# Kernel tuning notes

Hardware: AMD Instinct MI355X
Metric: run time of the kernel (lower is better)

Reference implementation:

```python
import jax, jax.numpy as jnp
import numpy as np

N_NODES = 8192
N_GRAPHS = 16
KNN_K = 80
N_FEAT = 6
KNN_COLS = (0, 1, 2, 3)
HID = 128
HID6 = 6 * HID
N_LABELS = 3
BN_EPS = 1e-5


def knn_edges(pos, batch, k):
    # pos: [N, 4]; batch: [N] graph ids. Returns (src, tgt) with k neighbors per node,
    # restricted to same graph, excluding self (PyG knn_graph, flow source_to_target).
    n = pos.shape[0]
    sq = jnp.sum(pos * pos, axis=1)
    d2 = sq[:, None] + sq[None, :] - 2.0 * (pos @ pos.T)  # [N, N]
    valid = (batch[:, None] == batch[None, :]) & ~jnp.eye(n, dtype=bool)
    d2 = jnp.where(valid, d2, jnp.inf)
    _, idx = jax.lax.top_k(-d2, k)  # k smallest distances per row
    src = idx.reshape(-1)                      # neighbor j (message source)
    tgt = jnp.repeat(jnp.arange(n), k)         # center node i (message target)
    return src, tgt


def tag_conv(x, src, tgt, norm, W, b):
    # TAGConv K=2: out = sum_k (A_hat^k x) W_k + b, A_hat = D^-1/2 A D^-1/2
    n = x.shape[0]
    out = x @ W[0]
    h = x
    for k in range(1, W.shape[0]):
        h = jax.ops.segment_sum(norm[:, None] * h[src], tgt, num_segments=n)
        out = out + h @ W[k]
    return out + b


def pool_mean_max(x, batch, n_graphs):
    cnt = jax.ops.segment_sum(jnp.ones((x.shape[0],), x.dtype), batch, num_segments=n_graphs)
    mean = jax.ops.segment_sum(x, batch, num_segments=n_graphs) / cnt[:, None]
    mx = jax.ops.segment_max(x, batch, num_segments=n_graphs)
    return jnp.concatenate([mean, mx], axis=1)


def setup_inputs() -> dict:
    key = jax.random.key(0)
    ks = jax.random.split(key, 16)
    x = jax.random.normal(ks[0], (N_NODES, N_FEAT), dtype=jnp.float32)
    batch = jnp.repeat(jnp.arange(N_GRAPHS, dtype=jnp.int32), N_NODES // N_GRAPHS)
    s1 = 1.0 / np.sqrt(N_FEAT)
    s2 = 1.0 / np.sqrt(HID)
    s3 = 1.0 / np.sqrt(HID6)
    return {
        "x": x,
        "batch": batch,
        "conv1_w": jax.random.uniform(ks[1], (3, N_FEAT, HID), jnp.float32, -s1, s1),
        "conv1_b": jnp.zeros((HID,), jnp.float32),
        "conv2_w": jax.random.uniform(ks[2], (3, HID, HID), jnp.float32, -s2, s2),
        "conv2_b": jnp.zeros((HID,), jnp.float32),
        "conv3_w": jax.random.uniform(ks[3], (3, HID, HID), jnp.float32, -s2, s2),
        "conv3_b": jnp.zeros((HID,), jnp.float32),
        "bn_gamma": jnp.ones((HID6,), jnp.float32),
        "bn_beta": jnp.zeros((HID6,), jnp.float32),
        "bn_mean": 0.1 * jax.random.normal(ks[4], (HID6,), jnp.float32),
        "bn_var": jax.random.uniform(ks[5], (HID6,), jnp.float32, 0.5, 1.5),
        "lin_w": jax.random.uniform(ks[6], (5, HID6, HID6), jnp.float32, -s3, s3),
        "lin_b": jax.random.uniform(ks[7], (5, HID6), jnp.float32, -s3, s3),
        "out_w": jax.random.uniform(ks[8], (HID6, N_LABELS), jnp.float32, -s3, s3),
        "out_b": jax.random.uniform(ks[9], (N_LABELS,), jnp.float32, -s3, s3),
    }


def reference(x, batch, conv1_w, conv1_b, conv2_w, conv2_b, conv3_w, conv3_b,
              bn_gamma, bn_beta, bn_mean, bn_var, lin_w, lin_b, out_w, out_b):
    n = x.shape[0]
    pos = x[:, jnp.array(KNN_COLS)]
    src, tgt = knn_edges(pos, batch, KNN_K)
    # gcn_norm without self loops (edge dropout disabled: eval-mode determinism)
    deg = jax.ops.segment_sum(jnp.ones_like(src, dtype=x.dtype), tgt, num_segments=n)
    dinv = jnp.where(deg > 0, jax.lax.rsqrt(jnp.maximum(deg, 1.0)), 0.0)
    norm = dinv[src] * dinv[tgt]

    h = jax.nn.leaky_relu(tag_conv(x, src, tgt, norm, conv1_w, conv1_b))
    p1 = pool_mean_max(h, batch, N_GRAPHS)
    h = jax.nn.leaky_relu(tag_conv(h, src, tgt, norm, conv2_w, conv2_b))
    p2 = pool_mean_max(h, batch, N_GRAPHS)
    h = jax.nn.leaky_relu(tag_conv(h, src, tgt, norm, conv3_w, conv3_b))
    p3 = pool_mean_max(h, batch, N_GRAPHS)

    g = jnp.concatenate([p1, p2, p3], axis=1)  # [B, 768]
    g = (g - bn_mean) * jax.lax.rsqrt(bn_var + BN_EPS) * bn_gamma + bn_beta
    for i in range(lin_w.shape[0]):
        g = jax.nn.leaky_relu(g @ lin_w[i] + lin_b[i])
    out = g @ out_w + out_b
    return out.reshape(-1, N_LABELS)
```

## Files before the change

kernel.cpp:

```cpp
#include <hip/hip_runtime.h>

constexpr int N    = 8192;
constexpr int NPG  = 512;
constexpr int NG   = 16;
constexpr int KNN  = 80;
constexpr int F0   = 6;
constexpr int HID  = 128;
constexpr int H6   = 768;
constexpr int RPB  = 16;
constexpr int BPGR = NPG / RPB;

__device__ __forceinline__ float leaky(float v) { return v > 0.0f ? v : 0.01f * v; }

__device__ __forceinline__ int lanes_below(unsigned long long m) {
    return __builtin_amdgcn_mbcnt_hi((unsigned)(m >> 32),
           __builtin_amdgcn_mbcnt_lo((unsigned)m, 0));
}

__device__ __forceinline__ int wave_count_sum(int c) {
    int total = 0;
    #pragma unroll
    for (int b = 0; b < 4; b++)
        total += (int)__popcll(__ballot((c >> b) & 1)) << b;
    return total;
}

__global__ __launch_bounds__(256) void knn_kernel(const float* __restrict__ x,
                                                  int* __restrict__ nbr) {
    constexpr int BPG = 128;
    const int tid  = threadIdx.x;
    const int lane = tid & 63;
    const int wv   = tid >> 6;
    const int base = (blockIdx.x / BPG) << 9;
    const int t    = base + (blockIdx.x & (BPG - 1)) * 4 + wv;
    const int tl   = t - base;

    __shared__ float px[512], py[512], pz[512], pw[512];
    __shared__ unsigned long long skey[4 * 128];

    for (int j = tid; j < 512; j += 256) {
        const float* row = x + (size_t)(base + j) * F0;
        const float2 ra = *(const float2*)(row);
        const float2 rb = *(const float2*)(row + 2);
        px[j] = ra.x; py[j] = ra.y; pz[j] = rb.x; pw[j] = rb.y;
    }
    __syncthreads();

    const float tx = px[tl], ty = py[tl], tz = pz[tl], tw = pw[tl];
    const float sqt = tx*tx + ty*ty + tz*tz + tw*tw;

    unsigned d2m[8];
    #pragma unroll
    for (int j = 0; j < 8; j++) {
        const int node = j * 64 + lane;
        const float jx = px[node], jy = py[node], jz = pz[node], jw = pw[node];
        const float sqj = jx*jx + jy*jy + jz*jz + jw*jw;
        const float dot = tx*jx + ty*jy + tz*jz + tw*jw;
        const float d2  = sqt + sqj - 2.0f * dot;
        unsigned u = __float_as_uint(d2);
        u = (u & 0x80000000u) ? ~u : (u | 0x80000000u);
        d2m[j] = (node == tl) ? 0xFFFFFFFFu : u;
    }

    unsigned V = 0;
    for (int b = 31; b >= 0; --b) {
        const unsigned test = V | (1u << b);
        int c = 0;
        #pragma unroll
        for (int j = 0; j < 8; j++) c += (d2m[j] < test) ? 1 : 0;
        if (wave_count_sum(c) < KNN) V = test;
    }

    int c = 0;
    #pragma unroll
    for (int j = 0; j < 8; j++) c += (d2m[j] < V) ? 1 : 0;
    const int n_lt = wave_count_sum(c);
    const int need = KNN - n_lt;

    const int woff = wv * 128;
    int cnt_total = 0, taken = 0;
    #pragma unroll
    for (int j = 0; j < 8; j++) {
        const bool lt = d2m[j] < V;
        const bool eq = d2m[j] == V;
        const unsigned long long meq = __ballot(eq);
        const bool sel = lt || (eq && (taken + lanes_below(meq)) < need);
        taken += (int)__popcll(meq);
        const unsigned long long msel = __ballot(sel);
        if (sel) {
            const int pos = cnt_total + lanes_below(msel);
            skey[woff + pos] = ((unsigned long long)d2m[j] << 32)
                             | (unsigned)(base + j * 64 + lane);
        }
        cnt_total += (int)__popcll(msel);
    }
    for (int i = KNN + lane; i < 128; i += 64) skey[woff + i] = ~0ULL;
    __syncthreads();

    for (int kk = 2; kk <= 128; kk <<= 1) {
        for (int jj = kk >> 1; jj >= 1; jj >>= 1) {
            const int i  = ((lane & ~(jj - 1)) << 1) | (lane & (jj - 1));
            const int ix = i | jj;
            const unsigned long long a = skey[woff + i];
            const unsigned long long b = skey[woff + ix];
            const bool up = ((i & kk) == 0);
            if ((a > b) == up) { skey[woff + i] = b; skey[woff + ix] = a; }
            __syncthreads();
        }
    }

    if (lane < KNN)      nbr[t * KNN + lane]      = (int)(unsigned)skey[woff + lane];
    if (lane + 64 < KNN) nbr[t * KNN + lane + 64] = (int)(unsigned)skey[woff + lane + 64];
}

__global__ __launch_bounds__(256) void prop6(const float* __restrict__ hin,
                                             const int* __restrict__ nbr,
                                             float* __restrict__ hout) {
    const int t = blockIdx.x * 256 + threadIdx.x;
    if (t >= N) return;
    const int* nb = nbr + t * KNN;
    float a0=0.f,a1=0.f,a2=0.f,a3=0.f,a4=0.f,a5=0.f;
    for (int i = 0; i < KNN; i += 4) {
        const int4 s4 = *(const int4*)(nb + i);
        {   const float* r = hin + (size_t)s4.x * F0;
            a0+=r[0]; a1+=r[1]; a2+=r[2]; a3+=r[3]; a4+=r[4]; a5+=r[5]; }
        {   const float* r = hin + (size_t)s4.y * F0;
            a0+=r[0]; a1+=r[1]; a2+=r[2]; a3+=r[3]; a4+=r[4]; a5+=r[5]; }
        {   const float* r = hin + (size_t)s4.z * F0;
            a0+=r[0]; a1+=r[1]; a2+=r[2]; a3+=r[3]; a4+=r[4]; a5+=r[5]; }
        {   const float* r = hin + (size_t)s4.w * F0;
            a0+=r[0]; a1+=r[1]; a2+=r[2]; a3+=r[3]; a4+=r[4]; a5+=r[5]; }
    }
    const float inv = 1.0f / 80.0f;
    float* o = hout + (size_t)t * F0;
    o[0]=a0*inv; o[1]=a1*inv; o[2]=a2*inv; o[3]=a3*inv; o[4]=a4*inv; o[5]=a5*inv;
}

__global__ __launch_bounds__(128) void prop128(const float* __restrict__ hin,
                                               const int* __restrict__ nbr,
                                               float* __restrict__ hout) {
    const int lane = threadIdx.x & 31;
    const int t    = blockIdx.x * 4 + (threadIdx.x >> 5);
    const int* nb  = nbr + t * KNN;
    float a0=0.f,a1=0.f,a2=0.f,a3=0.f;
    for (int i = 0; i < KNN; i += 16) {
        const int4 sA = *(const int4*)(nb + i);
        const int4 sB = *(const int4*)(nb + i + 4);
        const int4 sC = *(const int4*)(nb + i + 8);
        const int4 sD = *(const int4*)(nb + i + 12);
        const int idx[16] = {sA.x,sA.y,sA.z,sA.w, sB.x,sB.y,sB.z,sB.w,
                             sC.x,sC.y,sC.z,sC.w, sD.x,sD.y,sD.z,sD.w};
        float4 v[16];
        #pragma unroll
        for (int q = 0; q < 16; q++)
            v[q] = *(const float4*)(hin + (size_t)idx[q] * HID + lane * 4);
        #pragma unroll
        for (int q = 0; q < 16; q += 4) {
            a0 += (v[q].x + v[q+1].x) + (v[q+2].x + v[q+3].x);
            a1 += (v[q].y + v[q+1].y) + (v[q+2].y + v[q+3].y);
            a2 += (v[q].z + v[q+1].z) + (v[q+2].z + v[q+3].z);
            a3 += (v[q].w + v[q+1].w) + (v[q+2].w + v[q+3].w);
        }
    }
    const float inv = 1.0f / 80.0f;
    float4 r; r.x=a0*inv; r.y=a1*inv; r.z=a2*inv; r.w=a3*inv;
    *(float4*)(hout + (size_t)t * HID + lane * 4) = r;
}

template<int K>
__global__ __launch_bounds__(256) void combine_kernel(const float* __restrict__ X,
                                                      const float* __restrict__ Y1,
                                                      const float* __restrict__ Y2,
                                                      const float* __restrict__ W,
                                                      const float* __restrict__ bias,
                                                      float* __restrict__ out,
                                                      float* __restrict__ psum,
                                                      float* __restrict__ pmax) {
    __shared__ float xs[3][RPB * K];
    const int tid  = threadIdx.x;
    const int row0 = blockIdx.x * RPB;

    {
        const float* s0 = X  + (size_t)row0 * K;
        const float* s1 = Y1 + (size_t)row0 * K;
        const float* s2 = Y2 + (size_t)row0 * K;
        if constexpr ((K & 3) == 0) {
            constexpr int NV = RPB * K / 4;
            for (int i = tid; i < NV; i += 256) ((float4*)xs[0])[i] = ((const float4*)s0)[i];
            for (int i = tid; i < NV; i += 256) ((float4*)xs[1])[i] = ((const float4*)s1)[i];
            for (int i = tid; i < NV; i += 256) ((float4*)xs[2])[i] = ((const float4*)s2)[i];
        } else {
            for (int i = tid; i < RPB * K; i += 256) xs[0][i] = s0[i];
            for (int i = tid; i < RPB * K; i += 256) xs[1][i] = s1[i];
            for (int i = tid; i < RPB * K; i += 256) xs[2][i] = s2[i];
        }
    }
    __syncthreads();

    const int c  = tid & 127;
    const int r0 = (tid >> 7) * 8;

    float acc[8];
    #pragma unroll
    for (int r = 0; r < 8; r++) acc[r] = 0.0f;

    #pragma unroll
    for (int s = 0; s < 3; s++) {
        const float* __restrict__ Ws   = W + (size_t)s * K * HID;
        const float* __restrict__ xseg = xs[s] + r0 * K;
        for (int k = 0; k < K; k += 2) {
            const float w0 = Ws[(size_t)k * HID + c];
            const float w1 = Ws[(size_t)(k + 1) * HID + c];
            #pragma unroll
            for (int r = 0; r < 8; r++)
                acc[r] += xseg[r * K + k] * w0 + xseg[r * K + k + 1] * w1;
        }
    }

    const float bb = bias[c];
    float sum8 = 0.0f, mx8 = -3.402823e38f;
    #pragma unroll
    for (int r = 0; r < 8; r++) {
        const float v = leaky(acc[r] + bb);
        out[(size_t)(row0 + r0 + r) * HID + c] = v;
        sum8 += v;
        mx8 = fmaxf(mx8, v);
    }

    __shared__ float ssum[128], smx[128];
    if (r0) { ssum[c] = sum8; smx[c] = mx8; }
    __syncthreads();
    if (!r0) {
        psum[(size_t)blockIdx.x * HID + c] = sum8 + ssum[c];
        pmax[(size_t)blockIdx.x * HID + c] = fmaxf(mx8, smx[c]);
    }
}

__global__ __launch_bounds__(128) void pool2_kernel(const float* __restrict__ psum,
                                                    const float* __restrict__ pmax,
                                                    float* __restrict__ g, int conv) {
    const int gr = blockIdx.x;
    const int c  = threadIdx.x;
    float s = 0.0f, m = -3.402823e38f;
    const float* ps = psum + (size_t)gr * BPGR * HID + c;
    const float* pm = pmax + (size_t)gr * BPGR * HID + c;
    #pragma unroll 8
    for (int b = 0; b < BPGR; b++) {
        s += ps[b * HID];
        m = fmaxf(m, pm[b * HID]);
    }
    float* grow = g + (size_t)gr * H6 + conv * 256;
    grow[c]       = s * (1.0f / 512.0f);
    grow[128 + c] = m;
}

template<bool BN>
__global__ __launch_bounds__(256) void lin_kernel(const float* __restrict__ gin,
                                                  const float* __restrict__ W,
                                                  const float* __restrict__ bias,
                                                  float* __restrict__ gout,
                                                  const float* __restrict__ gamma,
                                                  const float* __restrict__ beta,
                                                  const float* __restrict__ mean,
                                                  const float* __restrict__ var) {
    const int r   = blockIdx.x / 6;
    const int cc  = blockIdx.x % 6;
    const int tid = threadIdx.x;

    __shared__ float gs[H6];
    for (int k = tid; k < H6; k += 256) {
        float v = gin[(size_t)r * H6 + k];
        if (BN) v = (v - mean[k]) * (1.0f / sqrtf(var[k] + 1e-5f)) * gamma[k] + beta[k];
        gs[k] = v;
    }
    __syncthreads();

    const int c  = cc * 128 + (tid & 127);
    const int kh = tid >> 7;
    const int kb = kh * 384;
    float a0=0.f,a1=0.f,a2=0.f,a3=0.f;
    for (int k = kb; k < kb + 384; k += 4) {
        a0 += gs[k]     * W[(size_t)(k)     * H6 + c];
        a1 += gs[k + 1] * W[(size_t)(k + 1) * H6 + c];
        a2 += gs[k + 2] * W[(size_t)(k + 2) * H6 + c];
        a3 += gs[k + 3] * W[(size_t)(k + 3) * H6 + c];
    }
    __shared__ float part[256];
    part[tid] = (a0 + a1) + (a2 + a3);
    __syncthreads();
    if (kh == 0) {
        const float v = part[tid] + part[tid + 128] + bias[c];
        gout[(size_t)r * H6 + c] = leaky(v);
    }
}

__global__ void out_kernel(const float* __restrict__ gin,
                           const float* __restrict__ W,
                           const float* __restrict__ bias,
                           float* __restrict__ out) {
    const int tid = threadIdx.x;
    __shared__ float part[192];
    if (tid < 192) {
        const int q  = tid >> 2;
        const int r  = q / 3, c = q % 3;
        const int kq = tid & 3;
        float acc = 0.0f;
        for (int k = kq * 192; k < kq * 192 + 192; k++)
            acc += gin[(size_t)r * H6 + k] * W[(size_t)k * 3 + c];
        part[tid] = acc;
    }
    __syncthreads();
    if (tid < 48) {
        const int r = tid / 3, c = tid % 3;
        out[r * 3 + c] = part[tid*4] + part[tid*4+1] + part[tid*4+2] + part[tid*4+3] + bias[c];
    }
}

extern "C" void kernel_launch(void* const* d_in, const int* in_sizes, int n_in,
                              void* d_out, int out_size, void* d_ws, size_t ws_size,
                              hipStream_t stream) {
    const float* x        = (const float*)d_in[0];
    const float* conv1_w  = (const float*)d_in[2];
    const float* conv1_b  = (const float*)d_in[3];
    const float* conv2_w  = (const float*)d_in[4];
    const float* conv2_b  = (const float*)d_in[5];
    const float* conv3_w  = (const float*)d_in[6];
    const float* conv3_b  = (const float*)d_in[7];
    const float* bn_gamma = (const float*)d_in[8];
    const float* bn_beta  = (const float*)d_in[9];
    const float* bn_mean  = (const float*)d_in[10];
    const float* bn_var   = (const float*)d_in[11];
    const float* lin_w    = (const float*)d_in[12];
    const float* lin_b    = (const float*)d_in[13];
    const float* out_w    = (const float*)d_in[14];
    const float* out_b    = (const float*)d_in[15];

    char* ws = (char*)d_ws;
    size_t off = 0;
    auto alloc = [&](size_t bytes) {
        void* p = ws + off;
        off += (bytes + 255) & ~(size_t)255;
        return p;
    };
    int*   nbr  = (int*)  alloc((size_t)N * KNN * 4);
    float* y6a  = (float*)alloc((size_t)N * F0 * 4);
    float* y6b  = (float*)alloc((size_t)N * F0 * 4);
    float* hA   = (float*)alloc((size_t)N * HID * 4);
    float* hB   = (float*)alloc((size_t)N * HID * 4);
    float* y1   = (float*)alloc((size_t)N * HID * 4);
    float* y2   = (float*)alloc((size_t)N * HID * 4);
    float* ga   = (float*)alloc((size_t)NG * H6 * 4);
    float* gb   = (float*)alloc((size_t)NG * H6 * 4);
    float* psum = (float*)alloc((size_t)(N / RPB) * HID * 4);
    float* pmax = (float*)alloc((size_t)(N / RPB) * HID * 4);

    knn_kernel<<<N / 4, 256, 0, stream>>>(x, nbr);

    prop6<<<N / 256, 256, 0, stream>>>(x, nbr, y6a);
    prop6<<<N / 256, 256, 0, stream>>>(y6a, nbr, y6b);
    combine_kernel<6><<<N / RPB, 256, 0, stream>>>(x, y6a, y6b, conv1_w, conv1_b, hA, psum, pmax);
    pool2_kernel<<<NG, 128, 0, stream>>>(psum, pmax, ga, 0);

    prop128<<<N / 4, 128, 0, stream>>>(hA, nbr, y1);
    prop128<<<N / 4, 128, 0, stream>>>(y1, nbr, y2);
    combine_kernel<128><<<N / RPB, 256, 0, stream>>>(hA, y1, y2, conv2_w, conv2_b, hB, psum, pmax);
    pool2_kernel<<<NG, 128, 0, stream>>>(psum, pmax, ga, 1);

    prop128<<<N / 4, 128, 0, stream>>>(hB, nbr, y1);
    prop128<<<N / 4, 128, 0, stream>>>(y1, nbr, y2);
    combine_kernel<128><<<N / RPB, 256, 0, stream>>>(hB, y1, y2, conv3_w, conv3_b, hA, psum, pmax);
    pool2_kernel<<<NG, 128, 0, stream>>>(psum, pmax, ga, 2);

    lin_kernel<true ><<<96, 256, 0, stream>>>(ga, lin_w + 0 * H6 * H6, lin_b + 0 * H6, gb,
                                              bn_gamma, bn_beta, bn_mean, bn_var);
    lin_kernel<false><<<96, 256, 0, stream>>>(gb, lin_w + 1 * H6 * H6, lin_b + 1 * H6, ga,
                                              nullptr, nullptr, nullptr, nullptr);
    lin_kernel<false><<<96, 256, 0, stream>>>(ga, lin_w + 2 * H6 * H6, lin_b + 2 * H6, gb,
                                              nullptr, nullptr, nullptr, nullptr);
    lin_kernel<false><<<96, 256, 0, stream>>>(gb, lin_w + 3 * H6 * H6, lin_b + 3 * H6, ga,
                                              nullptr, nullptr, nullptr, nullptr);
    lin_kernel<false><<<96, 256, 0, stream>>>(ga, lin_w + 4 * H6 * H6, lin_b + 4 * H6, gb,
                                              nullptr, nullptr, nullptr, nullptr);
    out_kernel<<<1, 256, 0, stream>>>(gb, out_w, out_b, (float*)d_out);
}
```

Measured before the change: 292.1 us.

## Replace gather-based 128-wide propagation with dense per-graph adjacency MFMA matmuls

The kNN kernel now also builds a dense fp16 0/1 adjacency matrix per graph (512x512 blocks). The 128-feature propagation hops become block-diagonal dense matmuls on MFMA, with features split into hi/lo fp16 pairs to keep near-fp32 accuracy. A split kernel transposes and splits features, and the first hop emits the split form of its output for the second hop. This trades irregular gathers for about 6x redundant dense FLOPs on the matrix cores, plus extra workspace and transposition traffic.

```diff
diff --git a/kernel.cpp b/kernel.cpp
--- a/kernel.cpp
+++ b/kernel.cpp
@@ -9,6 +9,10 @@
 constexpr int H6   = 768;
 constexpr int RPB  = 16;
 constexpr int BPGR = NPG / RPB;
+constexpr size_t SPLIT_STRIDE = (size_t)NG * HID * NPG;
+
+typedef _Float16 half8 __attribute__((ext_vector_type(8)));
+typedef float    f32x4 __attribute__((ext_vector_type(4)));
 
 __device__ __forceinline__ float leaky(float v) { return v > 0.0f ? v : 0.01f * v; }
 
@@ -26,7 +30,8 @@
 }
 
 __global__ __launch_bounds__(256) void knn_kernel(const float* __restrict__ x,
-                                                  int* __restrict__ nbr) {
+                                                  int* __restrict__ nbr,
+                                                  _Float16* __restrict__ Aadj) {
     constexpr int BPG = 128;
     const int tid  = threadIdx.x;
     const int lane = tid & 63;
@@ -37,6 +42,11 @@
 
     __shared__ float px[512], py[512], pz[512], pw[512];
     __shared__ unsigned long long skey[4 * 128];
+
+    {
+        const uint4 z = {0u, 0u, 0u, 0u};
+        *(uint4*)(Aadj + (size_t)t * 512 + lane * 8) = z;
+    }
 
     for (int j = tid; j < 512; j += 256) {
         const float* row = x + (size_t)(base + j) * F0;
@@ -109,8 +119,16 @@
         }
     }
 
-    if (lane < KNN)      nbr[t * KNN + lane]      = (int)(unsigned)skey[woff + lane];
-    if (lane + 64 < KNN) nbr[t * KNN + lane + 64] = (int)(unsigned)skey[woff + lane + 64];
+    if (lane < KNN) {
+        const int idx = (int)(unsigned)skey[woff + lane];
+        nbr[t * KNN + lane] = idx;
+        Aadj[(size_t)t * 512 + (idx & 511)] = (_Float16)1.0f;
+    }
+    if (lane + 64 < KNN) {
+        const int idx = (int)(unsigned)skey[woff + lane + 64];
+        nbr[t * KNN + lane + 64] = idx;
+        Aadj[(size_t)t * 512 + (idx & 511)] = (_Float16)1.0f;
+    }
 }
 
 __global__ __launch_bounds__(256) void prop6(const float* __restrict__ hin,
@@ -136,35 +154,141 @@
     o[0]=a0*inv; o[1]=a1*inv; o[2]=a2*inv; o[3]=a3*inv; o[4]=a4*inv; o[5]=a5*inv;
 }
 
-__global__ __launch_bounds__(128) void prop128(const float* __restrict__ hin,
-                                               const int* __restrict__ nbr,
-                                               float* __restrict__ hout) {
-    const int lane = threadIdx.x & 31;
-    const int t    = blockIdx.x * 4 + (threadIdx.x >> 5);
-    const int* nb  = nbr + t * KNN;
-    float a0=0.f,a1=0.f,a2=0.f,a3=0.f;
-    for (int i = 0; i < KNN; i += 16) {
-        const int4 sA = *(const int4*)(nb + i);
-        const int4 sB = *(const int4*)(nb + i + 4);
-        const int4 sC = *(const int4*)(nb + i + 8);
-        const int4 sD = *(const int4*)(nb + i + 12);
-        const int idx[16] = {sA.x,sA.y,sA.z,sA.w, sB.x,sB.y,sB.z,sB.w,
-                             sC.x,sC.y,sC.z,sC.w, sD.x,sD.y,sD.z,sD.w};
-        float4 v[16];
-        #pragma unroll
-        for (int q = 0; q < 16; q++)
-            v[q] = *(const float4*)(hin + (size_t)idx[q] * HID + lane * 4);
-        #pragma unroll
-        for (int q = 0; q < 16; q += 4) {
-            a0 += (v[q].x + v[q+1].x) + (v[q+2].x + v[q+3].x);
-            a1 += (v[q].y + v[q+1].y) + (v[q+2].y + v[q+3].y);
-            a2 += (v[q].z + v[q+1].z) + (v[q+2].z + v[q+3].z);
-            a3 += (v[q].w + v[q+1].w) + (v[q+2].w + v[q+3].w);
-        }
-    }
+__global__ __launch_bounds__(256) void split_kernel(const float* __restrict__ H,
+                                                    _Float16* __restrict__ Bout) {
+    __shared__ unsigned tt[128][67];
+    const int tid = threadIdx.x;
+    const int n0  = blockIdx.x * 64;
+    const int g   = n0 >> 9;
+    const int nl  = n0 & 511;
+
+    #pragma unroll
+    for (int q = 0; q < 8; q++) {
+        const int i  = tid + q * 256;
+        const int n  = i >> 5;
+        const int c4 = (i & 31) * 4;
+        const float4 v = *(const float4*)(H + ((size_t)(n0 + n)) * HID + c4);
+        const float fr[4] = {v.x, v.y, v.z, v.w};
+        #pragma unroll
+        for (int e = 0; e < 4; e++) {
+            const float f = fr[e];
+            const _Float16 h1 = (_Float16)f;
+            const _Float16 h2 = (_Float16)(f - (float)h1);
+            tt[c4 + e][n] = ((unsigned)__builtin_bit_cast(unsigned short, h2) << 16)
+                          |  (unsigned)__builtin_bit_cast(unsigned short, h1);
+        }
+    }
+    __syncthreads();
+
+    const int c  = tid >> 1;
+    const int jh = tid & 1;
+    _Float16 o1[32], o2[32];
+    #pragma unroll
+    for (int s = 0; s < 32; s++) {
+        const unsigned u = tt[c][jh * 32 + s];
+        o1[s] = __builtin_bit_cast(_Float16, (unsigned short)(u & 0xFFFFu));
+        o2[s] = __builtin_bit_cast(_Float16, (unsigned short)(u >> 16));
+    }
+    _Float16* d1 = Bout + ((size_t)g * HID + c) * NPG + nl + jh * 32;
+    _Float16* d2 = d1 + SPLIT_STRIDE;
+    #pragma unroll
+    for (int q = 0; q < 4; q++) {
+        *(uint4*)(d1 + q * 8) = *(const uint4*)&o1[q * 8];
+        *(uint4*)(d2 + q * 8) = *(const uint4*)&o2[q * 8];
+    }
+}
+
+template<bool EMIT>
+__global__ __launch_bounds__(128) void hop_kernel(const _Float16* __restrict__ A,
+                                                  const _Float16* __restrict__ Bin,
+                                                  float* __restrict__ Y,
+                                                  _Float16* __restrict__ Bout) {
+    __shared__ _Float16 Bs[2][128][72];
+    __shared__ float Ct[32][132];
+
+    const int tid  = threadIdx.x;
+    const int lane = tid & 63;
+    const int w    = tid >> 6;
+    const int g    = blockIdx.x >> 4;
+    const int m0   = (blockIdx.x & 15) * 32;
+
+    f32x4 acc[8];
+    #pragma unroll
+    for (int j = 0; j < 8; j++) acc[j] = {0.f, 0.f, 0.f, 0.f};
+
+    const _Float16* Arow = A + ((size_t)(g * 512 + m0 + w * 16 + (lane & 15))) * 512;
+    const int klane = (lane >> 4) * 8;
+    const int stg_c = tid >> 3;
+    const int stg_o = (tid & 7) * 8;
+
+    for (int ch = 0; ch < 8; ch++) {
+        const int k0 = ch * 64;
+        #pragma unroll
+        for (int s = 0; s < 2; s++) {
+            const _Float16* src = Bin + (size_t)s * SPLIT_STRIDE
+                                + (size_t)g * HID * NPG + k0;
+            #pragma unroll
+            for (int it = 0; it < 8; it++) {
+                const int cc = stg_c + it * 16;
+                const uint4 v = *(const uint4*)(src + (size_t)cc * NPG + stg_o);
+                *(uint4*)&Bs[s][cc][stg_o] = v;
+            }
+        }
+        __syncthreads();
+        #pragma unroll
+        for (int ks = 0; ks < 2; ks++) {
+            const half8 af = *(const half8*)(Arow + k0 + ks * 32 + klane);
+            #pragma unroll
+            for (int s = 0; s < 2; s++) {
+                #pragma unroll
+                for (int j = 0; j < 8; j++) {
+                    const half8 bf = *(const half8*)&Bs[s][j * 16 + (lane & 15)][ks * 32 + klane];
+                    acc[j] = __builtin_amdgcn_mfma_f32_16x16x32_f16(af, bf, acc[j], 0, 0, 0);
+                }
+            }
+        }
+        __syncthreads();
+    }
+
     const float inv = 1.0f / 80.0f;
-    float4 r; r.x=a0*inv; r.y=a1*inv; r.z=a2*inv; r.w=a3*inv;
-    *(float4*)(hout + (size_t)t * HID + lane * 4) = r;
+    {
+        const int rbase = w * 16 + (lane >> 4) * 4;
+        const int c0 = lane & 15;
+        #pragma unroll
+        for (int j = 0; j < 8; j++)
+            #pragma unroll
+            for (int rg = 0; rg < 4; rg++)
+                Ct[rbase + rg][j * 16 + c0] = acc[j][rg] * inv;
+    }
+    __syncthreads();
+
+    #pragma unroll
+    for (int q = 0; q < 8; q++) {
+        const int i  = tid + q * 128;
+        const int r  = i >> 5;
+        const int c4 = (i & 31) * 4;
+        const float4 v = *(const float4*)&Ct[r][c4];
+        *(float4*)(Y + ((size_t)(g * 512 + m0 + r)) * HID + c4) = v;
+    }
+
+    if (EMIT) {
+        const int c = tid;
+        _Float16 o1[32], o2[32];
+        #pragma unroll
+        for (int k = 0; k < 32; k++) {
+            const float v = Ct[k][c];
+            const _Float16 h1 = (_Float16)v;
+            o1[k] = h1;
+            o2[k] = (_Float16)(v - (float)h1);
+        }
+        _Float16* d1 = Bout + ((size_t)g * HID + c) * NPG + m0;
+        _Float16* d2 = d1 + SPLIT_STRIDE;
+        #pragma unroll
+        for (int q = 0; q < 4; q++) {
+            *(uint4*)(d1 + q * 8) = *(const uint4*)&o1[q * 8];
+            *(uint4*)(d2 + q * 8) = *(const uint4*)&o2[q * 8];
+        }
+    }
 }
 
 template<int K>
@@ -342,32 +466,37 @@
         off += (bytes + 255) & ~(size_t)255;
         return p;
     };
-    int*   nbr  = (int*)  alloc((size_t)N * KNN * 4);
-    float* y6a  = (float*)alloc((size_t)N * F0 * 4);
-    float* y6b  = (float*)alloc((size_t)N * F0 * 4);
-    float* hA   = (float*)alloc((size_t)N * HID * 4);
-    float* hB   = (float*)alloc((size_t)N * HID * 4);
-    float* y1   = (float*)alloc((size_t)N * HID * 4);
-    float* y2   = (float*)alloc((size_t)N * HID * 4);
-    float* ga   = (float*)alloc((size_t)NG * H6 * 4);
-    float* gb   = (float*)alloc((size_t)NG * H6 * 4);
-    float* psum = (float*)alloc((size_t)(N / RPB) * HID * 4);
-    float* pmax = (float*)alloc((size_t)(N / RPB) * HID * 4);
-
-    knn_kernel<<<N / 4, 256, 0, stream>>>(x, nbr);
+    int*      nbr  = (int*)      alloc((size_t)N * KNN * 4);
+    float*    y6a  = (float*)    alloc((size_t)N * F0 * 4);
+    float*    y6b  = (float*)    alloc((size_t)N * F0 * 4);
+    float*    hA   = (float*)    alloc((size_t)N * HID * 4);
+    float*    hB   = (float*)    alloc((size_t)N * HID * 4);
+    float*    y1   = (float*)    alloc((size_t)N * HID * 4);
+    float*    y2   = (float*)    alloc((size_t)N * HID * 4);
+    float*    ga   = (float*)    alloc((size_t)NG * H6 * 4);
+    float*    gb   = (float*)    alloc((size_t)NG * H6 * 4);
+    float*    psum = (float*)    alloc((size_t)(N / RPB) * HID * 4);
+    float*    pmax = (float*)    alloc((size_t)(N / RPB) * HID * 4);
+    _Float16* Aadj = (_Float16*) alloc((size_t)N * NPG * 2);
+    _Float16* Sa   = (_Float16*) alloc(2 * SPLIT_STRIDE * 2);
+    _Float16* Sb   = (_Float16*) alloc(2 * SPLIT_STRIDE * 2);
+
+    knn_kernel<<<N / 4, 256, 0, stream>>>(x, nbr, Aadj);
 
     prop6<<<N / 256, 256, 0, stream>>>(x, nbr, y6a);
     prop6<<<N / 256, 256, 0, stream>>>(y6a, nbr, y6b);
     combine_kernel<6><<<N / RPB, 256, 0, stream>>>(x, y6a, y6b, conv1_w, conv1_b, hA, psum, pmax);
     pool2_kernel<<<NG, 128, 0, stream>>>(psum, pmax, ga, 0);
 
-    prop128<<<N / 4, 128, 0, stream>>>(hA, nbr, y1);
-    prop128<<<N / 4, 128, 0, stream>>>(y1, nbr, y2);
+    split_kernel<<<N / 64, 256, 0, stream>>>(hA, Sa);
+    hop_kernel<true ><<<NG * 16, 128, 0, stream>>>(Aadj, Sa, y1, Sb);
+    hop_kernel<false><<<NG * 16, 128, 0, stream>>>(Aadj, Sb, y2, nullptr);
     combine_kernel<128><<<N / RPB, 256, 0, stream>>>(hA, y1, y2, conv2_w, conv2_b, hB, psum, pmax);
     pool2_kernel<<<NG, 128, 0, stream>>>(psum, pmax, ga, 1);
 
-    prop128<<<N / 4, 128, 0, stream>>>(hB, nbr, y1);
-    prop128<<<N / 4, 128, 0, stream>>>(y1, nbr, y2);
+    split_kernel<<<N / 64, 256, 0, stream>>>(hB, Sa);
+    hop_kernel<true ><<<NG * 16, 128, 0, stream>>>(Aadj, Sa, y1, Sb);
+    hop_kernel<false><<<NG * 16, 128, 0, stream>>>(Aadj, Sb, y2, nullptr);
     combine_kernel<128><<<N / RPB, 256, 0, stream>>>(hB, y1, y2, conv3_w, conv3_b, hA, psum, pmax);
     pool2_kernel<<<NG, 128, 0, stream>>>(psum, pmax, ga, 2);
 
```

New measurement: 307.5 us. 1.05x slower.

## Fuse conv1 per graph in shared memory and fold pooling into lin0

Applied to the files above, without the earlier changes.

Conv1's two 6-wide propagations, the combine and the mean/max pooling now run in a single per-graph kernel that keeps x, y1 and y2 in shared memory. It relies on neighbours being in the same 512-node graph, hence the index masking. The separate pool2 launches are removed and the conv2/conv3 partial pools are reduced inside the first linear layer. prop128 also moves to 256-thread blocks. The aim is fewer launches and less global traffic, but conv1 now runs on only 16 blocks, which limits parallelism.

```diff
diff --git a/kernel.cpp b/kernel.cpp
--- a/kernel.cpp
+++ b/kernel.cpp
@@ -113,34 +113,93 @@
     if (lane + 64 < KNN) nbr[t * KNN + lane + 64] = (int)(unsigned)skey[woff + lane + 64];
 }
 
-__global__ __launch_bounds__(256) void prop6(const float* __restrict__ hin,
-                                             const int* __restrict__ nbr,
-                                             float* __restrict__ hout) {
-    const int t = blockIdx.x * 256 + threadIdx.x;
-    if (t >= N) return;
-    const int* nb = nbr + t * KNN;
-    float a0=0.f,a1=0.f,a2=0.f,a3=0.f,a4=0.f,a5=0.f;
-    for (int i = 0; i < KNN; i += 4) {
-        const int4 s4 = *(const int4*)(nb + i);
-        {   const float* r = hin + (size_t)s4.x * F0;
-            a0+=r[0]; a1+=r[1]; a2+=r[2]; a3+=r[3]; a4+=r[4]; a5+=r[5]; }
-        {   const float* r = hin + (size_t)s4.y * F0;
-            a0+=r[0]; a1+=r[1]; a2+=r[2]; a3+=r[3]; a4+=r[4]; a5+=r[5]; }
-        {   const float* r = hin + (size_t)s4.z * F0;
-            a0+=r[0]; a1+=r[1]; a2+=r[2]; a3+=r[3]; a4+=r[4]; a5+=r[5]; }
-        {   const float* r = hin + (size_t)s4.w * F0;
-            a0+=r[0]; a1+=r[1]; a2+=r[2]; a3+=r[3]; a4+=r[4]; a5+=r[5]; }
-    }
-    const float inv = 1.0f / 80.0f;
-    float* o = hout + (size_t)t * F0;
-    o[0]=a0*inv; o[1]=a1*inv; o[2]=a2*inv; o[3]=a3*inv; o[4]=a4*inv; o[5]=a5*inv;
-}
-
-__global__ __launch_bounds__(128) void prop128(const float* __restrict__ hin,
+__global__ __launch_bounds__(256) void conv1_fused(const float* __restrict__ x,
+                                                   const int* __restrict__ nbr,
+                                                   const float* __restrict__ W,
+                                                   const float* __restrict__ bias,
+                                                   float* __restrict__ h,
+                                                   float* __restrict__ ga) {
+    __shared__ float xs[512][F0], y1s[512][F0], y2s[512][F0];
+    __shared__ float ssum[128], smx[128];
+    const int gr   = blockIdx.x;
+    const int base = gr << 9;
+    const int tid  = threadIdx.x;
+
+    for (int i = tid; i < 512 * F0; i += 256) ((float*)xs)[i] = x[(size_t)base * F0 + i];
+    __syncthreads();
+
+    for (int r = tid; r < 512; r += 256) {
+        const int* nb = nbr + (size_t)(base + r) * KNN;
+        float a0=0.f,a1=0.f,a2=0.f,a3=0.f,a4=0.f,a5=0.f;
+        for (int i = 0; i < KNN; i += 4) {
+            const int4 q = *(const int4*)(nb + i);
+            const int s0=q.x&511, s1=q.y&511, s2=q.z&511, s3=q.w&511;
+            a0 += (xs[s0][0]+xs[s1][0]) + (xs[s2][0]+xs[s3][0]);
+            a1 += (xs[s0][1]+xs[s1][1]) + (xs[s2][1]+xs[s3][1]);
+            a2 += (xs[s0][2]+xs[s1][2]) + (xs[s2][2]+xs[s3][2]);
+            a3 += (xs[s0][3]+xs[s1][3]) + (xs[s2][3]+xs[s3][3]);
+            a4 += (xs[s0][4]+xs[s1][4]) + (xs[s2][4]+xs[s3][4]);
+            a5 += (xs[s0][5]+xs[s1][5]) + (xs[s2][5]+xs[s3][5]);
+        }
+        const float inv = 1.0f / 80.0f;
+        y1s[r][0]=a0*inv; y1s[r][1]=a1*inv; y1s[r][2]=a2*inv;
+        y1s[r][3]=a3*inv; y1s[r][4]=a4*inv; y1s[r][5]=a5*inv;
+    }
+    __syncthreads();
+
+    for (int r = tid; r < 512; r += 256) {
+        const int* nb = nbr + (size_t)(base + r) * KNN;
+        float a0=0.f,a1=0.f,a2=0.f,a3=0.f,a4=0.f,a5=0.f;
+        for (int i = 0; i < KNN; i += 4) {
+            const int4 q = *(const int4*)(nb + i);
+            const int s0=q.x&511, s1=q.y&511, s2=q.z&511, s3=q.w&511;
+            a0 += (y1s[s0][0]+y1s[s1][0]) + (y1s[s2][0]+y1s[s3][0]);
+            a1 += (y1s[s0][1]+y1s[s1][1]) + (y1s[s2][1]+y1s[s3][1]);
+            a2 += (y1s[s0][2]+y1s[s1][2]) + (y1s[s2][2]+y1s[s3][2]);
+            a3 += (y1s[s0][3]+y1s[s1][3]) + (y1s[s2][3]+y1s[s3][3]);
+            a4 += (y1s[s0][4]+y1s[s1][4]) + (y1s[s2][4]+y1s[s3][4]);
+            a5 += (y1s[s0][5]+y1s[s1][5]) + (y1s[s2][5]+y1s[s3][5]);
+        }
+        const float inv = 1.0f / 80.0f;
+        y2s[r][0]=a0*inv; y2s[r][1]=a1*inv; y2s[r][2]=a2*inv;
+        y2s[r][3]=a3*inv; y2s[r][4]=a4*inv; y2s[r][5]=a5*inv;
+    }
+    __syncthreads();
+
+    const int c  = tid & 127;
+    const int rh = tid >> 7;
+    float w0[F0], w1[F0], w2[F0];
+    #pragma unroll
+    for (int f = 0; f < F0; f++) {
+        w0[f] = W[f * HID + c];
+        w1[f] = W[(F0 + f) * HID + c];
+        w2[f] = W[(2 * F0 + f) * HID + c];
+    }
+    const float bb = bias[c];
+    float psumv = 0.0f, pmaxv = -3.402823e38f;
+    for (int r = rh * 256; r < rh * 256 + 256; r++) {
+        float acc = bb;
+        #pragma unroll
+        for (int f = 0; f < F0; f++)
+            acc += xs[r][f] * w0[f] + y1s[r][f] * w1[f] + y2s[r][f] * w2[f];
+        acc = leaky(acc);
+        h[(size_t)(base + r) * HID + c] = acc;
+        psumv += acc;
+        pmaxv = fmaxf(pmaxv, acc);
+    }
+    if (rh) { ssum[c] = psumv; smx[c] = pmaxv; }
+    __syncthreads();
+    if (!rh) {
+        ga[(size_t)gr * H6 + c]       = (psumv + ssum[c]) * (1.0f / 512.0f);
+        ga[(size_t)gr * H6 + 128 + c] = fmaxf(pmaxv, smx[c]);
+    }
+}
+
+__global__ __launch_bounds__(256) void prop128(const float* __restrict__ hin,
                                                const int* __restrict__ nbr,
                                                float* __restrict__ hout) {
     const int lane = threadIdx.x & 31;
-    const int t    = blockIdx.x * 4 + (threadIdx.x >> 5);
+    const int t    = blockIdx.x * 8 + (threadIdx.x >> 5);
     const int* nb  = nbr + t * KNN;
     float a0=0.f,a1=0.f,a2=0.f,a3=0.f;
     for (int i = 0; i < KNN; i += 16) {
@@ -184,16 +243,10 @@
         const float* s0 = X  + (size_t)row0 * K;
         const float* s1 = Y1 + (size_t)row0 * K;
         const float* s2 = Y2 + (size_t)row0 * K;
-        if constexpr ((K & 3) == 0) {
-            constexpr int NV = RPB * K / 4;
-            for (int i = tid; i < NV; i += 256) ((float4*)xs[0])[i] = ((const float4*)s0)[i];
-            for (int i = tid; i < NV; i += 256) ((float4*)xs[1])[i] = ((const float4*)s1)[i];
-            for (int i = tid; i < NV; i += 256) ((float4*)xs[2])[i] = ((const float4*)s2)[i];
-        } else {
-            for (int i = tid; i < RPB * K; i += 256) xs[0][i] = s0[i];
-            for (int i = tid; i < RPB * K; i += 256) xs[1][i] = s1[i];
-            for (int i = tid; i < RPB * K; i += 256) xs[2][i] = s2[i];
-        }
+        constexpr int NV = RPB * K / 4;
+        for (int i = tid; i < NV; i += 256) ((float4*)xs[0])[i] = ((const float4*)s0)[i];
+        for (int i = tid; i < NV; i += 256) ((float4*)xs[1])[i] = ((const float4*)s1)[i];
+        for (int i = tid; i < NV; i += 256) ((float4*)xs[2])[i] = ((const float4*)s2)[i];
     }
     __syncthreads();
 
@@ -236,43 +289,69 @@
     }
 }
 
-__global__ __launch_bounds__(128) void pool2_kernel(const float* __restrict__ psum,
-                                                    const float* __restrict__ pmax,
-                                                    float* __restrict__ g, int conv) {
-    const int gr = blockIdx.x;
-    const int c  = threadIdx.x;
-    float s = 0.0f, m = -3.402823e38f;
-    const float* ps = psum + (size_t)gr * BPGR * HID + c;
-    const float* pm = pmax + (size_t)gr * BPGR * HID + c;
-    #pragma unroll 8
-    for (int b = 0; b < BPGR; b++) {
-        s += ps[b * HID];
-        m = fmaxf(m, pm[b * HID]);
-    }
-    float* grow = g + (size_t)gr * H6 + conv * 256;
-    grow[c]       = s * (1.0f / 512.0f);
-    grow[128 + c] = m;
-}
-
-template<bool BN>
+__global__ __launch_bounds__(256) void lin0_kernel(const float* __restrict__ ga,
+                                                   const float* __restrict__ psum2,
+                                                   const float* __restrict__ pmax2,
+                                                   const float* __restrict__ psum3,
+                                                   const float* __restrict__ pmax3,
+                                                   const float* __restrict__ gamma,
+                                                   const float* __restrict__ beta,
+                                                   const float* __restrict__ mean,
+                                                   const float* __restrict__ var,
+                                                   const float* __restrict__ W,
+                                                   const float* __restrict__ bias,
+                                                   float* __restrict__ gout) {
+    const int r   = blockIdx.x / 6;
+    const int cc  = blockIdx.x % 6;
+    const int tid = threadIdx.x;
+
+    __shared__ float gs[H6];
+    {
+        const int c  = tid & 127;
+        const int cv = tid >> 7;
+        const float* ps = (cv ? psum3 : psum2) + (size_t)r * BPGR * HID + c;
+        const float* pm = (cv ? pmax3 : pmax2) + (size_t)r * BPGR * HID + c;
+        float s = 0.0f, m = -3.402823e38f;
+        #pragma unroll 8
+        for (int b = 0; b < BPGR; b++) { s += ps[b * HID]; m = fmaxf(m, pm[b * HID]); }
+        gs[256 + cv * 256 + c]       = s * (1.0f / 512.0f);
+        gs[256 + cv * 256 + 128 + c] = m;
+        gs[tid] = ga[(size_t)r * H6 + tid];
+    }
+    __syncthreads();
+    for (int k = tid; k < H6; k += 256)
+        gs[k] = (gs[k] - mean[k]) * (1.0f / sqrtf(var[k] + 1e-5f)) * gamma[k] + beta[k];
+    __syncthreads();
+
+    const int c  = cc * 128 + (tid & 127);
+    const int kh = tid >> 7;
+    const int kb = kh * 384;
+    float a0=0.f,a1=0.f,a2=0.f,a3=0.f;
+    for (int k = kb; k < kb + 384; k += 4) {
+        a0 += gs[k]     * W[(size_t)(k)     * H6 + c];
+        a1 += gs[k + 1] * W[(size_t)(k + 1) * H6 + c];
+        a2 += gs[k + 2] * W[(size_t)(k + 2) * H6 + c];
+        a3 += gs[k + 3] * W[(size_t)(k + 3) * H6 + c];
+    }
+    __shared__ float part[256];
+    part[tid] = (a0 + a1) + (a2 + a3);
+    __syncthreads();
+    if (kh == 0) {
+        const float v = part[tid] + part[tid + 128] + bias[c];
+        gout[(size_t)r * H6 + c] = leaky(v);
+    }
+}
+
 __global__ __launch_bounds__(256) void lin_kernel(const float* __restrict__ gin,
                                                   const float* __restrict__ W,
                                                   const float* __restrict__ bias,
-                                                  float* __restrict__ gout,
-                                                  const float* __restrict__ gamma,
-                                                  const float* __restrict__ beta,
-                                                  const float* __restrict__ mean,
-                                                  const float* __restrict__ var) {
+                                                  float* __restrict__ gout) {
     const int r   = blockIdx.x / 6;
     const int cc  = blockIdx.x % 6;
     const int tid = threadIdx.x;
 
     __shared__ float gs[H6];
-    for (int k = tid; k < H6; k += 256) {
-        float v = gin[(size_t)r * H6 + k];
-        if (BN) v = (v - mean[k]) * (1.0f / sqrtf(var[k] + 1e-5f)) * gamma[k] + beta[k];
-        gs[k] = v;
-    }
+    for (int k = tid; k < H6; k += 256) gs[k] = gin[(size_t)r * H6 + k];
     __syncthreads();
 
     const int c  = cc * 128 + (tid & 127);
@@ -342,44 +421,36 @@
         off += (bytes + 255) & ~(size_t)255;
         return p;
     };
-    int*   nbr  = (int*)  alloc((size_t)N * KNN * 4);
-    float* y6a  = (float*)alloc((size_t)N * F0 * 4);
-    float* y6b  = (float*)alloc((size_t)N * F0 * 4);
-    float* hA   = (float*)alloc((size_t)N * HID * 4);
-    float* hB   = (float*)alloc((size_t)N * HID * 4);
-    float* y1   = (float*)alloc((size_t)N * HID * 4);
-    float* y2   = (float*)alloc((size_t)N * HID * 4);
-    float* ga   = (float*)alloc((size_t)NG * H6 * 4);
-    float* gb   = (float*)alloc((size_t)NG * H6 * 4);
-    float* psum = (float*)alloc((size_t)(N / RPB) * HID * 4);
-    float* pmax = (float*)alloc((size_t)(N / RPB) * HID * 4);
+    int*   nbr   = (int*)  alloc((size_t)N * KNN * 4);
+    float* hA    = (float*)alloc((size_t)N * HID * 4);
+    float* hB    = (float*)alloc((size_t)N * HID * 4);
+    float* y1    = (float*)alloc((size_t)N * HID * 4);
+    float* y2    = (float*)alloc((size_t)N * HID * 4);
+    float* ga    = (float*)alloc((size_t)NG * H6 * 4);
+    float* gb    = (float*)alloc((size_t)NG * H6 * 4);
+    float* psum2 = (float*)alloc((size_t)(N / RPB) * HID * 4);
+    float* pmax2 = (float*)alloc((size_t)(N / RPB) * HID * 4);
+    float* psum3 = (float*)alloc((size_t)(N / RPB) * HID * 4);
+    float* pmax3 = (float*)alloc((size_t)(N / RPB) * HID * 4);
 
     knn_kernel<<<N / 4, 256, 0, stream>>>(x, nbr);
 
-    prop6<<<N / 256, 256, 0, stream>>>(x, nbr, y6a);
-    prop6<<<N / 256, 256, 0, stream>>>(y6a, nbr, y6b);
-    combine_kernel<6><<<N / RPB, 256, 0, stream>>>(x, y6a, y6b, conv1_w, conv1_b, hA, psum, pmax);
-    pool2_kernel<<<NG, 128, 0, stream>>>(psum, pmax, ga, 0);
-
-    prop128<<<N / 4, 128, 0, stream>>>(hA, nbr, y1);
-    prop128<<<N / 4, 128, 0, stream>>>(y1, nbr, y2);
-    combine_kernel<128><<<N / RPB, 256, 0, stream>>>(hA, y1, y2, conv2_w, conv2_b, hB, psum, pmax);
-    pool2_kernel<<<NG, 128, 0, stream>>>(psum, pmax, ga, 1);
-
-    prop128<<<N / 4, 128, 0, stream>>>(hB, nbr, y1);
-    prop128<<<N / 4, 128, 0, stream>>>(y1, nbr, y2);
-    combine_kernel<128><<<N / RPB, 256, 0, stream>>>(hB, y1, y2, conv3_w, conv3_b, hA, psum, pmax);
-    pool2_kernel<<<NG, 128, 0, stream>>>(psum, pmax, ga, 2);
-
-    lin_kernel<true ><<<96, 256, 0, stream>>>(ga, lin_w + 0 * H6 * H6, lin_b + 0 * H6, gb,
-                                              bn_gamma, bn_beta, bn_mean, bn_var);
-    lin_kernel<false><<<96, 256, 0, stream>>>(gb, lin_w + 1 * H6 * H6, lin_b + 1 * H6, ga,
-                                              nullptr, nullptr, nullptr, nullptr);
-    lin_kernel<false><<<96, 256, 0, stream>>>(ga, lin_w + 2 * H6 * H6, lin_b + 2 * H6, gb,
-                                              nullptr, nullptr, nullptr, nullptr);
-    lin_kernel<false><<<96, 256, 0, stream>>>(gb, lin_w + 3 * H6 * H6, lin_b + 3 * H6, ga,
-                                              nullptr, nullptr, nullptr, nullptr);
-    lin_kernel<false><<<96, 256, 0, stream>>>(ga, lin_w + 4 * H6 * H6, lin_b + 4 * H6, gb,
-                                              nullptr, nullptr, nullptr, nullptr);
+    conv1_fused<<<NG, 256, 0, stream>>>(x, nbr, conv1_w, conv1_b, hA, ga);
+
+    prop128<<<N / 8, 256, 0, stream>>>(hA, nbr, y1);
+    prop128<<<N / 8, 256, 0, stream>>>(y1, nbr, y2);
+    combine_kernel<128><<<N / RPB, 256, 0, stream>>>(hA, y1, y2, conv2_w, conv2_b, hB, psum2, pmax2);
+
+    prop128<<<N / 8, 256, 0, stream>>>(hB, nbr, y1);
+    prop128<<<N / 8, 256, 0, stream>>>(y1, nbr, y2);
+    combine_kernel<128><<<N / RPB, 256, 0, stream>>>(hB, y1, y2, conv3_w, conv3_b, hA, psum3, pmax3);
+
+    lin0_kernel<<<96, 256, 0, stream>>>(ga, psum2, pmax2, psum3, pmax3,
+                                        bn_gamma, bn_beta, bn_mean, bn_var,
+                                        lin_w + 0 * H6 * H6, lin_b + 0 * H6, gb);
+    lin_kernel<<<96, 256, 0, stream>>>(gb, lin_w + 1 * H6 * H6, lin_b + 1 * H6, ga);
+    lin_kernel<<<96, 256, 0, stream>>>(ga, lin_w + 2 * H6 * H6, lin_b + 2 * H6, gb);
+    lin_kernel<<<96, 256, 0, stream>>>(gb, lin_w + 3 * H6 * H6, lin_b + 3 * H6, ga);
+    lin_kernel<<<96, 256, 0, stream>>>(ga, lin_w + 4 * H6 * H6, lin_b + 4 * H6, gb);
     out_kernel<<<1, 256, 0, stream>>>(gb, out_w, out_b, (float*)d_out);
 }
```

Result: slower. 310.4 us (+6.3%).
